# Performance work log

Measured on AMD Instinct MI355X. Metric: run time of the kernel, lower is better.

Reference implementation:

```python
import jax, jax.numpy as jnp
import numpy as np

B, F, D, A = 1024, 33, 128, 128  # batch, num_fields, embed_dim, attn_size (A must equal gnn dim)

def setup_inputs() -> dict:
    key = jax.random.key(0)
    k1, k2, k3, k4 = jax.random.split(key, 4)
    gnn_feature = jax.random.normal(k1, (B, A), dtype=jnp.float32)
    x = jax.random.normal(k2, (B, F, D), dtype=jnp.float32)
    # attention Linear(embed_dim -> attn_size): weight (A, D), bias (A,)
    lim = 1.0 / np.sqrt(D)
    attn_W = jax.random.uniform(k3, (A, D), minval=-lim, maxval=lim, dtype=jnp.float32)
    attn_b = jax.random.uniform(k4, (A,), minval=-lim, maxval=lim, dtype=jnp.float32)
    return {"gnn_feature": gnn_feature, "x": x, "attn_W": attn_W, "attn_b": attn_b}

def reference(gnn_feature, x, attn_W, attn_b):
    num_fields = x.shape[1]
    row, col = np.triu_indices(num_fields, k=1)  # P = F*(F-1)/2 pairs
    inner = x[:, row] * x[:, col]                # [B, P, D]
    fm = jax.nn.relu(jnp.einsum('bpd,ad->bpa', inner, attn_W) + attn_b)  # [B, P, A]
    # bmm(gnn[b,1,A], fm[b,p,A,1]) -> dot product per pair, softmax over pairs
    scores = jnp.einsum('ba,bpa->bp', gnn_feature, fm)  # [B, P]
    attn = jax.nn.softmax(scores, axis=1)               # [B, P]
    attn_output = jnp.einsum('bp,bpd->bd', attn, inner) * 100.0  # [B, D]
    return jnp.concatenate([gnn_feature, attn_output], axis=1)   # [B, A+D]
```

## Files before the change

### kernel.cpp

```cpp
#include <hip/hip_runtime.h>

#define FN 33
#define DN 128
#define AN 128
#define PN 528
#define XS 136
#define TS 36

typedef __attribute__((ext_vector_type(8))) _Float16 half8;
typedef __attribute__((ext_vector_type(4))) float f32x4;
typedef __attribute__((ext_vector_type(4))) unsigned int u32x4;

__device__ __forceinline__ unsigned int pkrtz(float a, float b) {
  return __builtin_bit_cast(unsigned int, __builtin_amdgcn_cvt_pkrtz(a, b));
}

__device__ __forceinline__ float row_max16(float v) {
  v = fmaxf(v, __builtin_bit_cast(float, __builtin_amdgcn_update_dpp(0, __builtin_bit_cast(int, v), 0x128, 0xF, 0xF, false)));
  v = fmaxf(v, __builtin_bit_cast(float, __builtin_amdgcn_update_dpp(0, __builtin_bit_cast(int, v), 0x124, 0xF, 0xF, false)));
  v = fmaxf(v, __builtin_bit_cast(float, __builtin_amdgcn_update_dpp(0, __builtin_bit_cast(int, v), 0x122, 0xF, 0xF, false)));
  v = fmaxf(v, __builtin_bit_cast(float, __builtin_amdgcn_update_dpp(0, __builtin_bit_cast(int, v), 0x121, 0xF, 0xF, false)));
  return v;
}

#define XLOAD(XV, XT, BB)                                                     \
  {                                                                           \
    const f32x4* xb = (const f32x4*)(xg + (size_t)(BB) * FN * DN);            \
    _Pragma("unroll")                                                         \
    for (int s = 0; s < 4; s++) {                                             \
      XV[s] = xb[tid + s * 256];                                              \
      asm volatile("" : "+v"(XV[s]));                                         \
    }                                                                         \
    if (tid < 32) XT = xb[1024 + tid];                                        \
    asm volatile("" : "+v"(XT));                                              \
  }

#define XSTORE(XV, XT, BUFI)                                                  \
  {                                                                           \
    _Pragma("unroll")                                                         \
    for (int s = 0; s < 4; s++) {                                             \
      const int idx = tid + s * 256;                                          \
      const int i = idx >> 5, d0 = (idx & 31) << 2;                           \
      *(uint2*)&xh[BUFI][i * XS + d0] =                                       \
          make_uint2(pkrtz(XV[s].x, XV[s].y), pkrtz(XV[s].z, XV[s].w));       \
    }                                                                         \
    if (tid < 32) {                                                           \
      const int idx = 1024 + tid;                                             \
      const int i = idx >> 5, d0 = (idx & 31) << 2;                           \
      *(uint2*)&xh[BUFI][i * XS + d0] =                                       \
          make_uint2(pkrtz(XT.x, XT.y), pkrtz(XT.z, XT.w));                   \
    }                                                                         \
  }

#define WALK(XHB, GQ, SPB, RMAXP)                                             \
  {                                                                           \
    const int t_beg = mh ? 17 : 0;                                            \
    const int t_end = mh ? 33 : 17;                                           \
    float wm = -3.4e38f;                                                      \
    unsigned int rc_next = rowcol[t_beg * 16 + u];                            \
    for (int t = t_beg; t < t_end; ++t) {                                     \
      const unsigned int rc = rc_next;                                        \
      if (t + 1 < t_end) rc_next = rowcol[(t + 1) * 16 + u];                  \
      const int r = rc & 255, c = rc >> 8;                                    \
      const _Float16* xr_base = &XHB[r * XS + q * 8];                         \
      const _Float16* xc_base = &XHB[c * XS + q * 8];                         \
      f32x4 acc[4];                                                           \
      _Pragma("unroll")                                                       \
      for (int nn = 0; nn < 4; nn++) acc[nn] = bq[nn];                        \
      __builtin_amdgcn_s_setprio(1);                                          \
      _Pragma("unroll")                                                       \
      for (int kk = 0; kk < 4; kk++) {                                        \
        half8 af = *(const half8*)(xr_base + kk * 32) *                       \
                   *(const half8*)(xc_base + kk * 32);                        \
        _Pragma("unroll")                                                     \
        for (int nn = 0; nn < 4; nn++)                                        \
          acc[nn] = __builtin_amdgcn_mfma_f32_16x16x32_f16(Bf[nn][kk], af,    \
                                                           acc[nn], 0, 0, 0);  \
      }                                                                       \
      __builtin_amdgcn_s_setprio(0);                                          \
      float sa0 = 0.f, sa1 = 0.f, sa2 = 0.f, sa3 = 0.f;                       \
      sa0 = fmaf(fmaxf(acc[0][0], 0.f), GQ[0].x, sa0);                        \
      sa0 = fmaf(fmaxf(acc[0][1], 0.f), GQ[0].y, sa0);                        \
      sa0 = fmaf(fmaxf(acc[0][2], 0.f), GQ[0].z, sa0);                        \
      sa0 = fmaf(fmaxf(acc[0][3], 0.f), GQ[0].w, sa0);                        \
      sa1 = fmaf(fmaxf(acc[1][0], 0.f), GQ[1].x, sa1);                        \
      sa1 = fmaf(fmaxf(acc[1][1], 0.f), GQ[1].y, sa1);                        \
      sa1 = fmaf(fmaxf(acc[1][2], 0.f), GQ[1].z, sa1);                        \
      sa1 = fmaf(fmaxf(acc[1][3], 0.f), GQ[1].w, sa1);                        \
      sa2 = fmaf(fmaxf(acc[2][0], 0.f), GQ[2].x, sa2);                        \
      sa2 = fmaf(fmaxf(acc[2][1], 0.f), GQ[2].y, sa2);                        \
      sa2 = fmaf(fmaxf(acc[2][2], 0.f), GQ[2].z, sa2);                        \
      sa2 = fmaf(fmaxf(acc[2][3], 0.f), GQ[2].w, sa2);                        \
      sa3 = fmaf(fmaxf(acc[3][0], 0.f), GQ[3].x, sa3);                        \
      sa3 = fmaf(fmaxf(acc[3][1], 0.f), GQ[3].y, sa3);                        \
      sa3 = fmaf(fmaxf(acc[3][2], 0.f), GQ[3].z, sa3);                        \
      sa3 = fmaf(fmaxf(acc[3][3], 0.f), GQ[3].w, sa3);                        \
      float s = (sa0 + sa1) + (sa2 + sa3);                                    \
      s += __shfl_xor(s, 16, 64);                  \
      wm = fmaxf(wm, s);                                                      \
      if ((q & 1) == 0)                                                       \
        SPB[(nh * 2 + (q >> 1)) * PN + t * 16 + u] = s;                       \
    }                                                                         \
    wm = row_max16(wm);                                                       \
    if (lane == 0)  RMAXP[wave * 2]     = wm;           \
    if (lane == 32) RMAXP[wave * 2 + 1] = wm;           \
  }

#define SPH(PARM)                                                             \
  {                                                                           \
    const float Mh =                                                          \
        (fmaxf(rmax[PARM][0], rmax[PARM][4]) +                                \
         fmaxf(rmax[PARM][1], rmax[PARM][5])) +                               \
        (fmaxf(rmax[PARM][2], rmax[PARM][6]) +                                \
         fmaxf(rmax[PARM][3], rmax[PARM][7]));                                \
    float s0 = (sp[PARM][0][tid] + sp[PARM][1][tid]) +                        \
               (sp[PARM][2][tid] + sp[PARM][3][tid]);                         \
    float s1 = (sp[PARM][0][tid + 256] + sp[PARM][1][tid + 256]) +            \
               (sp[PARM][2][tid + 256] + sp[PARM][3][tid + 256]);             \
    float e0 = __expf(s0 - Mh);                                               \
    float e1 = __expf(s1 - Mh);                                               \
    unsigned int rc = rowcol[tid];                                            \
    attn2d[PARM][(rc & 255) * TS + ((rc >> 8) - (rc & 255) - 1)] = e0;        \
    rc = rowcol[tid + 256];                                                   \
    attn2d[PARM][(rc & 255) * TS + ((rc >> 8) - (rc & 255) - 1)] = e1;        \
    float e2 = 0.f;                                                           \
    if (tid < 16) {                                                           \
      float s2 = (sp[PARM][0][tid + 512] + sp[PARM][1][tid + 512]) +          \
                 (sp[PARM][2][tid + 512] + sp[PARM][3][tid + 512]);           \
      e2 = __expf(s2 - Mh);                                                   \
      rc = rowcol[tid + 512];                                                 \
      attn2d[PARM][(rc & 255) * TS + ((rc >> 8) - (rc & 255) - 1)] = e2;      \
    }                                                                         \
    float ls = (e0 + e1) + e2;                                                \
    _Pragma("unroll")                                                         \
    for (int off = 32; off >= 1; off >>= 1) ls += __shfl_xor(ls, off, 64);    \
    if (lane == 0) rsum[PARM][wave] = ls;                                     \
  }

#define EPI(PARM, XHB)                                                        \
  {                                                                           \
    const int d = tid & 127;                                                  \
    const int h = tid >> 7;                                                   \
    float xcol[36];                                                           \
    _Pragma("unroll")                                                         \
    for (int i = 0; i < FN; i++) xcol[i] = (float)XHB[i * XS + d];            \
    xcol[33] = 0.f; xcol[34] = 0.f; xcol[35] = 0.f;                           \
    float accv = 0.f;                                                         \
    _Pragma("unroll")                                                         \
    for (int i = 0; i < 32; i++) {                                            \
      if ((i & 1) != h) continue;                                             \
      const int L = FN - 1 - i;                                               \
      const int nf4 = (L + 3) >> 2;                                           \
      float ti = 0.f;                                                         \
      _Pragma("unroll")                                                       \
      for (int t = 0; t < nf4; t++) {                                         \
        f32x4 a4 = *(const f32x4*)&attn2d[PARM][i * TS + t * 4];              \
        ti = fmaf(a4.x, xcol[i + 1 + t * 4 + 0], ti);                         \
        ti = fmaf(a4.y, xcol[i + 1 + t * 4 + 1], ti);                         \
        ti = fmaf(a4.z, xcol[i + 1 + t * 4 + 2], ti);                         \
        ti = fmaf(a4.w, xcol[i + 1 + t * 4 + 3], ti);                         \
      }                                                                       \
      accv = fmaf(xcol[i], ti, accv);                                         \
    }                                                                         \
    part[PARM][tid] = accv;                                                   \
  }

#define OUTW(PARM, BB)                                                        \
  if (tid < 128) {                                                            \
    const float Zb = (rsum[PARM][0] + rsum[PARM][1]) +                        \
                     (rsum[PARM][2] + rsum[PARM][3]);                         \
    float tot = part[PARM][tid] + part[PARM][tid + 128];                      \
    out[(size_t)(BB) * (AN + DN) + AN + tid] = tot * (100.0f / Zb);           \
  } else {                                                                    \
    const int a = tid - 128;                                                  \
    out[(size_t)(BB) * (AN + DN) + a] = gnn[(size_t)(BB) * AN + a];           \
  }

__global__ __launch_bounds__(256, 2)
void afm_kernel(const float* __restrict__ gnn, const float* __restrict__ xg,
                const float* __restrict__ Wg,  const float* __restrict__ bg,
                float* __restrict__ out)
{
  __shared__ __align__(16) _Float16 xh[2][FN * XS];
  __shared__ __align__(16) float attn2d[2][FN * TS];
  __shared__ __align__(16) float sp[2][4][PN];
  __shared__ __align__(16) float part[2][256];
  __shared__ unsigned short rowcol[PN];
  __shared__ float rmax[2][8], rsum[2][4];

  const int tid  = threadIdx.x;
  const int b0   = blockIdx.x * 2;
  const int b1   = b0 + 1;
  const int wave = tid >> 6;
  const int lane = tid & 63;
  const int q    = lane >> 4;
  const int u    = lane & 15;
  const int nh   = wave & 1;
  const int mh   = wave >> 1;

  f32x4 xv0[4], xv1[4];
  f32x4 xt0 = {0,0,0,0}, xt1 = {0,0,0,0};
  XLOAD(xv0, xt0, b0);
  XLOAD(xv1, xt1, b1);

  half8 Bf[4][4];
  f32x4 bq[4], g0q[4], g1q[4];
  #pragma unroll
  for (int nn = 0; nn < 4; nn++) {
    const int a = nh * 64 + nn * 16 + u;
    const float* src = Wg + (size_t)a * DN + q * 8;
    #pragma unroll
    for (int kk = 0; kk < 4; kk++) {
      f32x4 w0 = *(const f32x4*)(src + kk * 32);
      f32x4 w1 = *(const f32x4*)(src + kk * 32 + 4);
      u32x4 pk;
      pk.x = pkrtz(w0.x, w0.y);
      pk.y = pkrtz(w0.z, w0.w);
      pk.z = pkrtz(w1.x, w1.y);
      pk.w = pkrtz(w1.z, w1.w);
      Bf[nn][kk] = __builtin_bit_cast(half8, pk);
      asm volatile("" : "+v"(Bf[nn][kk]));
    }
    const int abase = nh * 64 + nn * 16 + q * 4;
    bq[nn]  = *(const f32x4*)&bg[abase];
    g0q[nn] = *(const f32x4*)&gnn[(size_t)b0 * AN + abase];
    g1q[nn] = *(const f32x4*)&gnn[(size_t)b1 * AN + abase];
    asm volatile("" : "+v"(bq[nn]), "+v"(g0q[nn]), "+v"(g1q[nn]));
  }

  {
    float* a2z = &attn2d[0][0];
    for (int idx = tid; idx < 2 * FN * TS; idx += 256) a2z[idx] = 0.0f;
    for (int p = tid; p < PN; p += 256) {
      int i = 0, rem = p;
      while (rem >= FN - 1 - i) { rem -= FN - 1 - i; i++; }
      rowcol[p] = (unsigned short)(i | ((i + 1 + rem) << 8));
    }
  }
  XSTORE(xv0, xt0, 0);
  XSTORE(xv1, xt1, 1);
  __syncthreads();

  WALK(xh[0], g0q, (&sp[0][0][0]), rmax[0]);
  __syncthreads();

  SPH(0);
  WALK(xh[1], g1q, (&sp[1][0][0]), rmax[1]);
  __syncthreads();

  SPH(1);
  EPI(0, xh[0]);
  __syncthreads();

  OUTW(0, b0);
  EPI(1, xh[1]);
  __syncthreads();

  OUTW(1, b1);
}

extern "C" void kernel_launch(void* const* d_in, const int* in_sizes, int n_in,
                              void* d_out, int out_size, void* d_ws, size_t ws_size,
                              hipStream_t stream) {
  (void)n_in; (void)out_size; (void)d_ws; (void)ws_size;
  const float* gnn  = (const float*)d_in[0];
  const float* x    = (const float*)d_in[1];
  const float* W    = (const float*)d_in[2];
  const float* bias = (const float*)d_in[3];
  float* out = (float*)d_out;
  const int Bn = in_sizes[0] / AN;
  afm_kernel<<<dim3(Bn / 2), dim3(256), 0, stream>>>(gnn, x, W, bias, out);
}
```

Before: 104.8 us.

## Interleave both batch walks in one MFMA loop and merge epilogues

The two per-batch score walks are fused into one loop that issues MFMAs for both batches in an interleaved way, sharing the row/col index loads and loop overhead while giving the MFMA pipeline two independent accumulator chains. The softmax phases for both batches then run back to back, and the epilogue maps half the threads to each batch so the whole weighted-sum step runs once over all i instead of twice over alternating halves. The shared part buffer and two barriers are removed, and the gnn passthrough is loaded early. In exchange, register pressure roughly doubles for accumulators in the walk, and each epilogue thread now does the full 32-row reduction.

```diff
diff --git a/kernel.cpp b/kernel.cpp
--- a/kernel.cpp
+++ b/kernel.cpp
@@ -52,58 +52,26 @@
     }                                                                         \
   }
 
-#define WALK(XHB, GQ, SPB, RMAXP)                                             \
-  {                                                                           \
-    const int t_beg = mh ? 17 : 0;                                            \
-    const int t_end = mh ? 33 : 17;                                           \
-    float wm = -3.4e38f;                                                      \
-    unsigned int rc_next = rowcol[t_beg * 16 + u];                            \
-    for (int t = t_beg; t < t_end; ++t) {                                     \
-      const unsigned int rc = rc_next;                                        \
-      if (t + 1 < t_end) rc_next = rowcol[(t + 1) * 16 + u];                  \
-      const int r = rc & 255, c = rc >> 8;                                    \
-      const _Float16* xr_base = &XHB[r * XS + q * 8];                         \
-      const _Float16* xc_base = &XHB[c * XS + q * 8];                         \
-      f32x4 acc[4];                                                           \
-      _Pragma("unroll")                                                       \
-      for (int nn = 0; nn < 4; nn++) acc[nn] = bq[nn];                        \
-      __builtin_amdgcn_s_setprio(1);                                          \
-      _Pragma("unroll")                                                       \
-      for (int kk = 0; kk < 4; kk++) {                                        \
-        half8 af = *(const half8*)(xr_base + kk * 32) *                       \
-                   *(const half8*)(xc_base + kk * 32);                        \
-        _Pragma("unroll")                                                     \
-        for (int nn = 0; nn < 4; nn++)                                        \
-          acc[nn] = __builtin_amdgcn_mfma_f32_16x16x32_f16(Bf[nn][kk], af,    \
-                                                           acc[nn], 0, 0, 0);  \
-      }                                                                       \
-      __builtin_amdgcn_s_setprio(0);                                          \
-      float sa0 = 0.f, sa1 = 0.f, sa2 = 0.f, sa3 = 0.f;                       \
-      sa0 = fmaf(fmaxf(acc[0][0], 0.f), GQ[0].x, sa0);                        \
-      sa0 = fmaf(fmaxf(acc[0][1], 0.f), GQ[0].y, sa0);                        \
-      sa0 = fmaf(fmaxf(acc[0][2], 0.f), GQ[0].z, sa0);                        \
-      sa0 = fmaf(fmaxf(acc[0][3], 0.f), GQ[0].w, sa0);                        \
-      sa1 = fmaf(fmaxf(acc[1][0], 0.f), GQ[1].x, sa1);                        \
-      sa1 = fmaf(fmaxf(acc[1][1], 0.f), GQ[1].y, sa1);                        \
-      sa1 = fmaf(fmaxf(acc[1][2], 0.f), GQ[1].z, sa1);                        \
-      sa1 = fmaf(fmaxf(acc[1][3], 0.f), GQ[1].w, sa1);                        \
-      sa2 = fmaf(fmaxf(acc[2][0], 0.f), GQ[2].x, sa2);                        \
-      sa2 = fmaf(fmaxf(acc[2][1], 0.f), GQ[2].y, sa2);                        \
-      sa2 = fmaf(fmaxf(acc[2][2], 0.f), GQ[2].z, sa2);                        \
-      sa2 = fmaf(fmaxf(acc[2][3], 0.f), GQ[2].w, sa2);                        \
-      sa3 = fmaf(fmaxf(acc[3][0], 0.f), GQ[3].x, sa3);                        \
-      sa3 = fmaf(fmaxf(acc[3][1], 0.f), GQ[3].y, sa3);                        \
-      sa3 = fmaf(fmaxf(acc[3][2], 0.f), GQ[3].z, sa3);                        \
-      sa3 = fmaf(fmaxf(acc[3][3], 0.f), GQ[3].w, sa3);                        \
-      float s = (sa0 + sa1) + (sa2 + sa3);                                    \
-      s += __shfl_xor(s, 16, 64);                  \
-      wm = fmaxf(wm, s);                                                      \
-      if ((q & 1) == 0)                                                       \
-        SPB[(nh * 2 + (q >> 1)) * PN + t * 16 + u] = s;                       \
-    }                                                                         \
-    wm = row_max16(wm);                                                       \
-    if (lane == 0)  RMAXP[wave * 2]     = wm;           \
-    if (lane == 32) RMAXP[wave * 2 + 1] = wm;           \
+#define RELUDOT(ACC, GQ, DST)                                                 \
+  {                                                                           \
+    float sa0 = 0.f, sa1 = 0.f, sa2 = 0.f, sa3 = 0.f;                         \
+    sa0 = fmaf(fmaxf(ACC[0][0], 0.f), GQ[0].x, sa0);                          \
+    sa0 = fmaf(fmaxf(ACC[0][1], 0.f), GQ[0].y, sa0);                          \
+    sa0 = fmaf(fmaxf(ACC[0][2], 0.f), GQ[0].z, sa0);                          \
+    sa0 = fmaf(fmaxf(ACC[0][3], 0.f), GQ[0].w, sa0);                          \
+    sa1 = fmaf(fmaxf(ACC[1][0], 0.f), GQ[1].x, sa1);                          \
+    sa1 = fmaf(fmaxf(ACC[1][1], 0.f), GQ[1].y, sa1);                          \
+    sa1 = fmaf(fmaxf(ACC[1][2], 0.f), GQ[1].z, sa1);                          \
+    sa1 = fmaf(fmaxf(ACC[1][3], 0.f), GQ[1].w, sa1);                          \
+    sa2 = fmaf(fmaxf(ACC[2][0], 0.f), GQ[2].x, sa2);                          \
+    sa2 = fmaf(fmaxf(ACC[2][1], 0.f), GQ[2].y, sa2);                          \
+    sa2 = fmaf(fmaxf(ACC[2][2], 0.f), GQ[2].z, sa2);                          \
+    sa2 = fmaf(fmaxf(ACC[2][3], 0.f), GQ[2].w, sa2);                          \
+    sa3 = fmaf(fmaxf(ACC[3][0], 0.f), GQ[3].x, sa3);                          \
+    sa3 = fmaf(fmaxf(ACC[3][1], 0.f), GQ[3].y, sa3);                          \
+    sa3 = fmaf(fmaxf(ACC[3][2], 0.f), GQ[3].z, sa3);                          \
+    sa3 = fmaf(fmaxf(ACC[3][3], 0.f), GQ[3].w, sa3);                          \
+    DST = (sa0 + sa1) + (sa2 + sa3);                                          \
   }
 
 #define SPH(PARM)                                                             \
@@ -137,45 +105,6 @@
     if (lane == 0) rsum[PARM][wave] = ls;                                     \
   }
 
-#define EPI(PARM, XHB)                                                        \
-  {                                                                           \
-    const int d = tid & 127;                                                  \
-    const int h = tid >> 7;                                                   \
-    float xcol[36];                                                           \
-    _Pragma("unroll")                                                         \
-    for (int i = 0; i < FN; i++) xcol[i] = (float)XHB[i * XS + d];            \
-    xcol[33] = 0.f; xcol[34] = 0.f; xcol[35] = 0.f;                           \
-    float accv = 0.f;                                                         \
-    _Pragma("unroll")                                                         \
-    for (int i = 0; i < 32; i++) {                                            \
-      if ((i & 1) != h) continue;                                             \
-      const int L = FN - 1 - i;                                               \
-      const int nf4 = (L + 3) >> 2;                                           \
-      float ti = 0.f;                                                         \
-      _Pragma("unroll")                                                       \
-      for (int t = 0; t < nf4; t++) {                                         \
-        f32x4 a4 = *(const f32x4*)&attn2d[PARM][i * TS + t * 4];              \
-        ti = fmaf(a4.x, xcol[i + 1 + t * 4 + 0], ti);                         \
-        ti = fmaf(a4.y, xcol[i + 1 + t * 4 + 1], ti);                         \
-        ti = fmaf(a4.z, xcol[i + 1 + t * 4 + 2], ti);                         \
-        ti = fmaf(a4.w, xcol[i + 1 + t * 4 + 3], ti);                         \
-      }                                                                       \
-      accv = fmaf(xcol[i], ti, accv);                                         \
-    }                                                                         \
-    part[PARM][tid] = accv;                                                   \
-  }
-
-#define OUTW(PARM, BB)                                                        \
-  if (tid < 128) {                                                            \
-    const float Zb = (rsum[PARM][0] + rsum[PARM][1]) +                        \
-                     (rsum[PARM][2] + rsum[PARM][3]);                         \
-    float tot = part[PARM][tid] + part[PARM][tid + 128];                      \
-    out[(size_t)(BB) * (AN + DN) + AN + tid] = tot * (100.0f / Zb);           \
-  } else {                                                                    \
-    const int a = tid - 128;                                                  \
-    out[(size_t)(BB) * (AN + DN) + a] = gnn[(size_t)(BB) * AN + a];           \
-  }
-
 __global__ __launch_bounds__(256, 2)
 void afm_kernel(const float* __restrict__ gnn, const float* __restrict__ xg,
                 const float* __restrict__ Wg,  const float* __restrict__ bg,
@@ -184,7 +113,6 @@
   __shared__ __align__(16) _Float16 xh[2][FN * XS];
   __shared__ __align__(16) float attn2d[2][FN * TS];
   __shared__ __align__(16) float sp[2][4][PN];
-  __shared__ __align__(16) float part[2][256];
   __shared__ unsigned short rowcol[PN];
   __shared__ float rmax[2][8], rsum[2][4];
 
@@ -202,6 +130,8 @@
   f32x4 xt0 = {0,0,0,0}, xt1 = {0,0,0,0};
   XLOAD(xv0, xt0, b0);
   XLOAD(xv1, xt1, b1);
+
+  const float gpass = gnn[(size_t)(b0 + (tid >> 7)) * AN + (tid & 127)];
 
   half8 Bf[4][4];
   f32x4 bq[4], g0q[4], g1q[4];
@@ -241,22 +171,93 @@
   XSTORE(xv1, xt1, 1);
   __syncthreads();
 
-  WALK(xh[0], g0q, (&sp[0][0][0]), rmax[0]);
+  {
+    const int t_beg = mh ? 17 : 0;
+    const int t_end = mh ? 33 : 17;
+    float wm0 = -3.4e38f, wm1 = -3.4e38f;
+    unsigned int rc_next = rowcol[t_beg * 16 + u];
+    for (int t = t_beg; t < t_end; ++t) {
+      const unsigned int rc = rc_next;
+      if (t + 1 < t_end) rc_next = rowcol[(t + 1) * 16 + u];
+      const int off_r = (rc & 255) * XS + q * 8;
+      const int off_c = (rc >> 8) * XS + q * 8;
+
+      f32x4 a0[4], a1[4];
+      #pragma unroll
+      for (int nn = 0; nn < 4; nn++) { a0[nn] = bq[nn]; a1[nn] = bq[nn]; }
+
+      __builtin_amdgcn_s_setprio(1);
+      #pragma unroll
+      for (int kk = 0; kk < 4; kk++) {
+        half8 af0 = *(const half8*)&xh[0][off_r + kk * 32] *
+                    *(const half8*)&xh[0][off_c + kk * 32];
+        half8 af1 = *(const half8*)&xh[1][off_r + kk * 32] *
+                    *(const half8*)&xh[1][off_c + kk * 32];
+        #pragma unroll
+        for (int nn = 0; nn < 4; nn++) {
+          a0[nn] = __builtin_amdgcn_mfma_f32_16x16x32_f16(Bf[nn][kk], af0, a0[nn], 0, 0, 0);
+          a1[nn] = __builtin_amdgcn_mfma_f32_16x16x32_f16(Bf[nn][kk], af1, a1[nn], 0, 0, 0);
+        }
+      }
+      __builtin_amdgcn_s_setprio(0);
+
+      float s0, s1;
+      RELUDOT(a0, g0q, s0);
+      RELUDOT(a1, g1q, s1);
+      s0 += __shfl_xor(s0, 16, 64);
+      s1 += __shfl_xor(s1, 16, 64);
+      wm0 = fmaxf(wm0, s0);
+      wm1 = fmaxf(wm1, s1);
+      if ((q & 1) == 0) {
+        const int gidx = (nh * 2 + (q >> 1)) * PN + t * 16 + u;
+        (&sp[0][0][0])[gidx] = s0;
+        (&sp[1][0][0])[gidx] = s1;
+      }
+    }
+    wm0 = row_max16(wm0);
+    wm1 = row_max16(wm1);
+    if (lane == 0)  { rmax[0][wave * 2]     = wm0; rmax[1][wave * 2]     = wm1; }
+    if (lane == 32) { rmax[0][wave * 2 + 1] = wm0; rmax[1][wave * 2 + 1] = wm1; }
+  }
   __syncthreads();
 
   SPH(0);
-  WALK(xh[1], g1q, (&sp[1][0][0]), rmax[1]);
+  SPH(1);
   __syncthreads();
 
-  SPH(1);
-  EPI(0, xh[0]);
-  __syncthreads();
-
-  OUTW(0, b0);
-  EPI(1, xh[1]);
-  __syncthreads();
-
-  OUTW(1, b1);
+  {
+    const int bi = tid >> 7;
+    const int d  = tid & 127;
+    const _Float16* xhb = &xh[bi][0];
+    const float* a2 = &attn2d[bi][0];
+    const float Zb = (rsum[bi][0] + rsum[bi][1]) + (rsum[bi][2] + rsum[bi][3]);
+
+    float xcol[36];
+    #pragma unroll
+    for (int i = 0; i < FN; i++) xcol[i] = (float)xhb[i * XS + d];
+    xcol[33] = 0.f; xcol[34] = 0.f; xcol[35] = 0.f;
+
+    float acc0 = 0.f, acc1 = 0.f;
+    #pragma unroll
+    for (int i = 0; i < 32; i++) {
+      const int L = FN - 1 - i;
+      const int nf4 = (L + 3) >> 2;
+      float ti = 0.f;
+      #pragma unroll
+      for (int t = 0; t < nf4; t++) {
+        f32x4 a4 = *(const f32x4*)&a2[i * TS + t * 4];
+        ti = fmaf(a4.x, xcol[i + 1 + t * 4 + 0], ti);
+        ti = fmaf(a4.y, xcol[i + 1 + t * 4 + 1], ti);
+        ti = fmaf(a4.z, xcol[i + 1 + t * 4 + 2], ti);
+        ti = fmaf(a4.w, xcol[i + 1 + t * 4 + 3], ti);
+      }
+      if (i & 1) acc1 = fmaf(xcol[i], ti, acc1);
+      else       acc0 = fmaf(xcol[i], ti, acc0);
+    }
+    const size_t obase = (size_t)(b0 + bi) * (AN + DN);
+    out[obase + AN + d] = (acc0 + acc1) * (100.0f / Zb);
+    out[obase + d] = gpass;
+  }
 }
 
 extern "C" void kernel_launch(void* const* d_in, const int* in_sizes, int n_in,
```

After: 101.3 us, median of 2. 3.4% less time.
